# Kernel optimization log

Measured on AMD Instinct MI355X. Metric: run time of the kernel, lower is better.

## Reference

```python
import jax, jax.numpy as jnp
import numpy as np

N_NODES = 50000
N_EDGES = 800000
IN, N1, N2, N3, N4, N5, L, NC = 7, 128, 128, 64, 64, 16, 16, 3


def _gat_params(key, fin, fout, edge_dim=1):
    ks = jax.random.split(key, 6)
    s = 0.1
    return dict(
        W=jax.random.normal(ks[0], (fin, fout), jnp.float32) * s,
        a_src=jax.random.normal(ks[1], (fout,), jnp.float32) * s,
        a_dst=jax.random.normal(ks[2], (fout,), jnp.float32) * s,
        We=jax.random.normal(ks[3], (edge_dim, fout), jnp.float32) * s,
        a_e=jax.random.normal(ks[4], (fout,), jnp.float32) * s,
        b=jax.random.normal(ks[5], (fout,), jnp.float32) * s,
    )


def setup_inputs() -> dict:
    key = jax.random.key(0)
    ks = jax.random.split(key, 16)
    inp = {
        'x1': jax.random.normal(ks[0], (N_NODES, IN), jnp.float32),
        'x2': jax.random.normal(ks[1], (N_NODES, IN), jnp.float32),
        'edge_index1': jax.random.randint(ks[2], (2, N_EDGES), 0, N_NODES),
        'edge_index2': jax.random.randint(ks[3], (2, N_EDGES), 0, N_NODES),
        'x_norm2_1': jax.random.normal(ks[4], (L,), jnp.float32),
        'x_norm2_2': jax.random.normal(ks[5], (L,), jnp.float32),
        'edge_col1': jax.random.uniform(ks[6], (N_EDGES, 1), jnp.float32),
        'edge_col2': jax.random.uniform(ks[7], (N_EDGES, 1), jnp.float32),
    }
    p1 = _gat_params(ks[8], IN, N1)
    p2 = _gat_params(ks[9], N1, N2)
    p3 = _gat_params(ks[10], N2, N3)
    for i, p in enumerate((p1, p2, p3), 1):
        for k, v in p.items():
            inp[f'{k}{i}'] = v
    s = 0.1
    inp['W_lin'] = jax.random.normal(ks[11], (N3 + L, N4), jnp.float32) * s
    inp['b_lin'] = jnp.zeros((N4,), jnp.float32)
    inp['W_c1'] = jax.random.normal(ks[12], (2 * N4, N5), jnp.float32) * s
    inp['b_c1'] = jnp.zeros((N5,), jnp.float32)
    inp['W_c2'] = jax.random.normal(ks[13], (N5, NC), jnp.float32) * s
    inp['b_c2'] = jnp.zeros((NC,), jnp.float32)
    return inp


def _gat_conv(x, src, dst, eattr, W, a_src, a_dst, We, a_e, b, n):
    # PyG GATConv, heads=1, add_self_loops with fill_value='mean'
    h = x @ W                                           # [N, C]
    ones = jnp.ones_like(dst, dtype=eattr.dtype)
    deg = jax.ops.segment_sum(ones, dst, n)
    loop_attr = jax.ops.segment_sum(eattr, dst, n) / jnp.maximum(deg, 1.0)[:, None]
    ar = jnp.arange(n, dtype=src.dtype)
    s = jnp.concatenate([src, ar])
    d = jnp.concatenate([dst, ar])
    ea = jnp.concatenate([eattr, loop_attr], axis=0)    # [E+N, edge_dim]
    alpha = (h @ a_src)[s] + (h @ a_dst)[d] + (ea @ We) @ a_e
    alpha = jax.nn.leaky_relu(alpha, 0.2)
    amax = jax.ops.segment_max(alpha, d, n)             # every node has a self loop
    ex = jnp.exp(alpha - amax[d])
    denom = jax.ops.segment_sum(ex, d, n)
    w = ex / denom[d]                                   # segment softmax weights
    out = jax.ops.segment_sum(w[:, None] * h[s], d, n)  # [N, C]
    return out + b


def _process_graph(x, ei, eattr, params):
    src, dst = ei[0], ei[1]
    n = x.shape[0]
    for p in params:
        x = jax.nn.elu(_gat_conv(x, src, dst, eattr, *p, n))
    return x.mean(axis=0)


def reference(x1, x2, edge_index1, edge_index2, x_norm2_1, x_norm2_2,
              edge_col1, edge_col2,
              W1, a_src1, a_dst1, We1, a_e1, b1,
              W2, a_src2, a_dst2, We2, a_e2, b2,
              W3, a_src3, a_dst3, We3, a_e3, b3,
              W_lin, b_lin, W_c1, b_c1, W_c2, b_c2):
    params = [
        (W1, a_src1, a_dst1, We1, a_e1, b1),
        (W2, a_src2, a_dst2, We2, a_e2, b2),
        (W3, a_src3, a_dst3, We3, a_e3, b3),
    ]
    g1 = _process_graph(x1, edge_index1, edge_col1, params)
    g2 = _process_graph(x2, edge_index2, edge_col2, params)
    g1 = jnp.concatenate([g1, x_norm2_1]) @ W_lin + b_lin
    g2 = jnp.concatenate([g2, x_norm2_2]) @ W_lin + b_lin
    x = jnp.concatenate([g1, g2])                       # [2*N4]
    h = jax.nn.relu(x @ W_c1 + b_c1)
    logits = h @ W_c2 + b_c2
    return logits[None, :]                              # [1, num_classes]
```

## Files before the change

### kernel.cpp

```cpp
#include <hip/hip_runtime.h>
#include <math.h>

#define NN 50000
#define NE 800000
#define NT 100000
#define NTP 100032
#define ET (2*NE + NT)
#define NPB 256
#define NB 391
#define BCH 4096
#define BCAP 5120

typedef __attribute__((ext_vector_type(8))) short bf16x8;
typedef __attribute__((ext_vector_type(4))) float f32x4;

static __device__ __forceinline__ float wave_max64(float v){
  #pragma unroll
  for(int off=32;off;off>>=1) v = fmaxf(v, __shfl_xor(v,off));
  return v;
}
static __device__ __forceinline__ float wave_sum64(float v){
  #pragma unroll
  for(int off=32;off;off>>=1) v += __shfl_xor(v,off);
  return v;
}
static __device__ __forceinline__ unsigned short f2bf(float f){
  unsigned u = __float_as_uint(f);
  return (unsigned short)((u + 0x7FFFu + ((u>>16)&1u)) >> 16);
}
static __device__ __forceinline__ float bflo(unsigned v){ return __uint_as_float(v<<16); }
static __device__ __forceinline__ float bfhi(unsigned v){ return __uint_as_float(v & 0xFFFF0000u); }

__global__ __launch_bounds__(256) void k_hist(const int* __restrict__ d1,
    const int* __restrict__ d2, int* __restrict__ bcnt){
  __shared__ int h[512];
  int t = threadIdx.x;
  h[t] = 0; h[t+256] = 0;
  __syncthreads();
  int stride = gridDim.x*256;
  for (int e = blockIdx.x*256 + t; e < NE; e += stride){
    atomicAdd(&h[d1[e]>>8], 1);
    atomicAdd(&h[(d2[e]+NN)>>8], 1);
  }
  __syncthreads();
  if (h[t])     atomicAdd(&bcnt[t],     h[t]);
  if (h[t+256]) atomicAdd(&bcnt[t+256], h[t+256]);
}

__global__ void k_hscan(const int* __restrict__ bcnt, int* __restrict__ hbase,
                        int* __restrict__ row_ptr){
  int t = threadIdx.x;
  int a = bcnt[2*t], b2 = bcnt[2*t+1];
  int s = a + b2;
  int lane = t & 63, wv = t >> 6;
  int inc = s;
  #pragma unroll
  for (int off=1; off<64; off<<=1){ int u = __shfl_up(inc, off); if (lane>=off) inc += u; }
  __shared__ int wsum[4];
  if (lane==63) wsum[wv] = inc;
  __syncthreads();
  int woff = 0;
  #pragma unroll
  for (int w=0; w<4; ++w) if (w < wv) woff += wsum[w];
  int excl = woff + inc - s;
  hbase[2*t] = excl; hbase[2*t+1] = excl + a;
  if (t==0) row_ptr[NT] = ET;
}

__global__ __launch_bounds__(256) void k_bin(const int* __restrict__ s1,
    const int* __restrict__ d1, const float* __restrict__ e1,
    const int* __restrict__ s2, const int* __restrict__ d2,
    const float* __restrict__ e2, const int* __restrict__ hbase,
    int* __restrict__ gcur, uint2* __restrict__ gstage){
  __shared__ int cnt[512], loff[512], cur[512], gbase_sh[512];
  __shared__ uint2 sdata[BCH];
  __shared__ unsigned short sbkt[BCH];
  __shared__ int wsum[4];
  int tid = threadIdx.x;
  int e0 = blockIdx.x*BCH;
  unsigned pack[16], eab[16];
  unsigned short bk[16];
  cnt[tid] = 0; cnt[tid+256] = 0; cur[tid] = 0; cur[tid+256] = 0;
  __syncthreads();
  #pragma unroll
  for (int u=0; u<16; ++u){
    int e = e0 + u*256 + tid;
    int b = NB; unsigned p = 0, ea = 0;
    if (e < 2*NE){
      int src, dst; float eav;
      if (e < NE){ src = s1[e]; dst = d1[e]; eav = e1[e]; }
      else { int e2i = e - NE; src = s2[e2i] + NN; dst = d2[e2i] + NN; eav = e2[e2i]; }
      b = dst >> 8;
      p = (unsigned)src | ((unsigned)(dst & 255) << 17);
      ea = __float_as_uint(eav);
    }
    bk[u] = (unsigned short)b; pack[u] = p; eab[u] = ea;
    atomicAdd(&cnt[b], 1);
  }
  __syncthreads();
  {
    int a = cnt[2*tid], b2 = cnt[2*tid+1];
    int s = a + b2;
    int lane = tid & 63, wv = tid >> 6;
    int inc = s;
    #pragma unroll
    for (int off=1; off<64; off<<=1){ int u = __shfl_up(inc, off); if (lane>=off) inc += u; }
    if (lane==63) wsum[wv] = inc;
    __syncthreads();
    int woff = 0;
    #pragma unroll
    for (int w=0; w<4; ++w) if (w < wv) woff += wsum[w];
    int excl = woff + inc - s;
    loff[2*tid] = excl; loff[2*tid+1] = excl + a;
  }
  if (tid < NB && cnt[tid] > 0)
    gbase_sh[tid] = hbase[tid] + atomicAdd(&gcur[tid], cnt[tid]);
  if (tid+256 < NB && cnt[tid+256] > 0)
    gbase_sh[tid+256] = hbase[tid+256] + atomicAdd(&gcur[tid+256], cnt[tid+256]);
  __syncthreads();
  #pragma unroll
  for (int u=0; u<16; ++u){
    int b = bk[u];
    int p = loff[b] + atomicAdd(&cur[b], 1);
    sdata[p] = make_uint2(pack[u], eab[u]);
    sbkt[p] = (unsigned short)b;
  }
  __syncthreads();
  for (int k = tid; k < BCH; k += 256){
    int b = sbkt[k];
    if (b < NB) gstage[gbase_sh[b] + (k - loff[b])] = sdata[k];
  }
}

__global__ __launch_bounds__(256) void k_bucket(const uint2* __restrict__ gstage,
    const int* __restrict__ hbase, int2* __restrict__ srt, int* __restrict__ row_ptr){
  __shared__ uint2 sd[BCAP];
  __shared__ int deg[256], rbase[256], cur[256];
  __shared__ float easum[256];
  __shared__ int wsum[4];
  int b = blockIdx.x, t = threadIdx.x;
  int lo = b*NPB;
  int nloc = min(NPB, NT - lo);
  int est = hbase[b], ecnt = hbase[b+1] - est;
  bool inlds = (ecnt <= BCAP);
  deg[t] = 0; easum[t] = 0.f;
  __syncthreads();
  for (int k = t; k < ecnt; k += 256){
    uint2 v = gstage[est + k];
    if (inlds) sd[k] = v;
    int dl = v.x >> 17;
    atomicAdd(&deg[dl], 1);
    atomicAdd(&easum[dl], __uint_as_float(v.y));
  }
  __syncthreads();
  int dv = (t < nloc) ? deg[t] + 1 : 0;
  int lane = t & 63, wv = t >> 6;
  int inc = dv;
  #pragma unroll
  for (int off=1; off<64; off<<=1){ int u = __shfl_up(inc, off); if (lane>=off) inc += u; }
  if (lane==63) wsum[wv] = inc;
  __syncthreads();
  int woff = 0;
  #pragma unroll
  for (int w=0; w<4; ++w) if (w < wv) woff += wsum[w];
  int gb = est + lo + (woff + inc - dv);
  if (t < nloc){
    row_ptr[lo + t] = gb;
    rbase[t] = gb;
    cur[t] = 1;
    float se = easum[t] / fmaxf((float)deg[t], 1.f);
    srt[gb] = make_int2(lo + t, __float_as_int(se));
  }
  __syncthreads();
  for (int k = t; k < ecnt; k += 256){
    uint2 v = inlds ? sd[k] : gstage[est + k];
    int dl = v.x >> 17;
    int pos = rbase[dl] + atomicAdd(&cur[dl], 1);
    srt[pos] = make_int2((int)(v.x & 0x1FFFFu), (int)v.y);
  }
}

__global__ __launch_bounds__(256) void k_prep(
    const float* __restrict__ We0, const float* __restrict__ ae0,
    const float* __restrict__ We1, const float* __restrict__ ae1,
    const float* __restrict__ We2, const float* __restrict__ ae2,
    float* __restrict__ ce3,
    const float* __restrict__ W1, const float* __restrict__ W2,
    unsigned short* __restrict__ Wt1, unsigned short* __restrict__ Wt2){
  int t = threadIdx.x;
  if (t < 64){
    const float* We[3] = {We0, We1, We2};
    const float* ae[3] = {ae0, ae1, ae2};
    const int fo[3] = {128, 128, 64};
    for (int L = 0; L < 3; ++L){
      float s = 0.f;
      for (int c = t; c < fo[L]; c += 64) s += We[L][c]*ae[L][c];
      s = wave_sum64(s);
      if (t == 0) ce3[L] = s;
    }
  }
  for (int i = t; i < 128*128; i += 256){
    int c = i >> 7, k = i & 127;
    Wt1[c*136 + k] = f2bf(W1[k*128 + c]);
  }
  for (int i = t; i < 64*128; i += 256){
    int c = i >> 7, k = i & 127;
    Wt2[c*136 + k] = f2bf(W2[k*64 + c]);
  }
}

template<int N>
__global__ __launch_bounds__(256) void k_gemm_mfma(
    const unsigned short* __restrict__ x16, const unsigned short* __restrict__ Wt,
    const float* __restrict__ a_src, const float* __restrict__ a_dst,
    unsigned short* __restrict__ h16, float* __restrict__ hs,
    float* __restrict__ hd, int n){
  constexpr int CT = N/16;
  __shared__ unsigned short Wl[N*136];
  int tid = threadIdx.x;
  for (int i = tid; i < N*136/8; i += 256)
    ((uint4*)Wl)[i] = ((const uint4*)Wt)[i];
  __syncthreads();
  int lane = tid & 63, w = tid >> 6;
  int arow = blockIdx.x*64 + w*16 + (lane & 15);
  int kb   = (lane >> 4) * 8;
  int rsafe = (arow < n) ? arow : (n-1);
  f32x4 acc[CT] = {};
  #pragma unroll
  for (int s = 0; s < 4; ++s){
    bf16x8 a = *(const bf16x8*)(x16 + (size_t)rsafe*128 + s*32 + kb);
    #pragma unroll
    for (int c = 0; c < CT; ++c){
      bf16x8 b = *(const bf16x8*)(&Wl[(c*16 + (lane&15))*136 + s*32 + kb]);
      acc[c] = __builtin_amdgcn_mfma_f32_16x16x32_bf16(a, b, acc[c], 0, 0, 0);
    }
  }
  int drow = blockIdx.x*64 + w*16 + (lane>>4)*4;
  int dcol = lane & 15;
  float psv[4] = {0,0,0,0}, pdv[4] = {0,0,0,0};
  #pragma unroll
  for (int c = 0; c < CT; ++c){
    float as = a_src[c*16 + dcol], ad = a_dst[c*16 + dcol];
    #pragma unroll
    for (int j = 0; j < 4; ++j){
      float v = acc[c][j];
      if (drow + j < n) h16[(size_t)(drow+j)*N + c*16 + dcol] = f2bf(v);
      psv[j] += v*as; pdv[j] += v*ad;
    }
  }
  #pragma unroll
  for (int off = 1; off < 16; off <<= 1){
    #pragma unroll
    for (int j=0;j<4;j++){ psv[j] += __shfl_xor(psv[j], off); pdv[j] += __shfl_xor(pdv[j], off); }
  }
  if (dcol == 0){
    #pragma unroll
    for (int j=0;j<4;j++) if (drow+j < n){ hs[drow+j] = psv[j]; hd[drow+j] = pdv[j]; }
  }
}

__global__ __launch_bounds__(256) void k_gemm7(const float* __restrict__ x1,
    const float* __restrict__ x2, const float* __restrict__ W,
    const float* __restrict__ a_src, const float* __restrict__ a_dst,
    unsigned short* __restrict__ h16, float* __restrict__ hs,
    float* __restrict__ hd, int n){
  __shared__ float Wl[7][128];
  int tid = threadIdx.x;
  for (int i = tid; i < 7*128; i += 256) ((float*)Wl)[i] = W[i];
  __syncthreads();
  int tx = tid & 31, ty = tid >> 5;
  int r = blockIdx.x*8 + ty;
  if (r >= n) return;
  const float* xr = (r < NN) ? (x1 + (size_t)r*7) : (x2 + (size_t)(r-NN)*7);
  float xv[7];
  #pragma unroll
  for (int k=0;k<7;k++) xv[k] = xr[k];
  float4 s = make_float4(0.f,0.f,0.f,0.f);
  #pragma unroll
  for (int k=0;k<7;k++){
    float4 wv = *(const float4*)(&Wl[k][tx*4]);
    s.x += xv[k]*wv.x; s.y += xv[k]*wv.y; s.z += xv[k]*wv.z; s.w += xv[k]*wv.w;
  }
  unsigned r0p = (unsigned)f2bf(s.x) | ((unsigned)f2bf(s.y)<<16);
  unsigned r1p = (unsigned)f2bf(s.z) | ((unsigned)f2bf(s.w)<<16);
  *(uint2*)(h16 + (size_t)r*128 + tx*4) = make_uint2(r0p, r1p);
  float ps = s.x*a_src[tx*4] + s.y*a_src[tx*4+1] + s.z*a_src[tx*4+2] + s.w*a_src[tx*4+3];
  float pd = s.x*a_dst[tx*4] + s.y*a_dst[tx*4+1] + s.z*a_dst[tx*4+2] + s.w*a_dst[tx*4+3];
  #pragma unroll
  for (int off=16; off; off>>=1){ ps += __shfl_xor(ps, off); pd += __shfl_xor(pd, off); }
  if (tx==0){ hs[r] = ps; hd[r] = pd; }
}

template<int FOUT, bool OBF>
__global__ __launch_bounds__(256) void k_aggregate(const unsigned short* __restrict__ h16,
    const float* __restrict__ hs, const float* __restrict__ hd,
    const int2* __restrict__ srt, const int* __restrict__ row_ptr,
    const float* __restrict__ ce_p, const float* __restrict__ b,
    void* __restrict__ xout, int n){
  constexpr int LPE = FOUT/8;
  constexpr int EPS = 64/LPE;
  __shared__ float s_p[4][64];
  __shared__ int   s_s[4][64];
  int tid = threadIdx.x;
  int wv = tid >> 6, lane = tid & 63;
  int wid = (int)((blockIdx.x*256 + tid) >> 6);
  if (wid >= n) return;
  float ce  = *ce_p;
  int beg = row_ptr[wid], end = row_ptr[wid+1];
  float hdn = hd[wid];
  int e_sub = lane / LPE;
  int col8  = (lane % LPE) * 8;
  float m = -INFINITY, den = 0.f;
  float acc[8] = {0.f,0.f,0.f,0.f,0.f,0.f,0.f,0.f};
  for (int base = beg; base < end; base += 64){
    int slot = base + lane;
    float a = -INFINITY; int src = 0;
    if (slot < end){
      int2 pk = srt[slot];
      src = pk.x;
      a = hs[src] + hdn + __int_as_float(pk.y)*ce;
      a = (a > 0.f) ? a : 0.2f*a;
    }
    float cm = wave_max64(a);
    float mnew = fmaxf(m, cm);
    float scale = __expf(m - mnew);
    den *= scale;
    #pragma unroll
    for (int u=0;u<8;u++) acc[u] *= scale;
    float p = __expf(a - mnew);
    den += wave_sum64(p);
    s_p[wv][lane] = p; s_s[wv][lane] = src;
    asm volatile("s_waitcnt lgkmcnt(0)" ::: "memory");
    int cnt = end - base; if (cnt > 64) cnt = 64;
    for (int j = 0; j < cnt; j += EPS){
      int jj = j + e_sub;
      float p0 = s_p[wv][jj];  int sj = s_s[wv][jj];
      uint4 h0 = *(const uint4*)(h16 + (size_t)sj*FOUT + col8);
      acc[0] += p0*bflo(h0.x); acc[1] += p0*bfhi(h0.x);
      acc[2] += p0*bflo(h0.y); acc[3] += p0*bfhi(h0.y);
      acc[4] += p0*bflo(h0.z); acc[5] += p0*bfhi(h0.z);
      acc[6] += p0*bflo(h0.w); acc[7] += p0*bfhi(h0.w);
    }
    m = mnew;
  }
  #pragma unroll
  for (int off = LPE; off < 64; off <<= 1){
    #pragma unroll
    for (int u=0;u<8;u++) acc[u] += __shfl_xor(acc[u], off);
  }
  float inv = 1.f/den;
  if (lane < LPE){
    float o[8];
    #pragma unroll
    for (int u=0;u<8;u++){
      o[u] = acc[u]*inv + b[col8+u];
      o[u] = (o[u] > 0.f) ? o[u] : (__expf(o[u]) - 1.f);
    }
    if (OBF){
      uint4 pkd;
      pkd.x = (unsigned)f2bf(o[0]) | ((unsigned)f2bf(o[1])<<16);
      pkd.y = (unsigned)f2bf(o[2]) | ((unsigned)f2bf(o[3])<<16);
      pkd.z = (unsigned)f2bf(o[4]) | ((unsigned)f2bf(o[5])<<16);
      pkd.w = (unsigned)f2bf(o[6]) | ((unsigned)f2bf(o[7])<<16);
      *(uint4*)((unsigned short*)xout + (size_t)wid*FOUT + col8) = pkd;
    } else {
      float4 o0 = make_float4(o[0],o[1],o[2],o[3]);
      float4 o1 = make_float4(o[4],o[5],o[6],o[7]);
      *(float4*)((float*)xout + (size_t)wid*FOUT + col8)     = o0;
      *(float4*)((float*)xout + (size_t)wid*FOUT + col8 + 4) = o1;
    }
  }
}

__global__ __launch_bounds__(256) void k_colsum2(const float* __restrict__ x,
    float* __restrict__ gsum, int n){
  __shared__ float ls[128];
  int t = threadIdx.x;
  if (t < 128) ls[t] = 0.f;
  __syncthreads();
  int c4 = (t & 15) * 4;
  int rsub = t >> 4;
  float4 s1 = make_float4(0.f,0.f,0.f,0.f), s2 = make_float4(0.f,0.f,0.f,0.f);
  for (int r = blockIdx.x*16 + rsub; r < n; r += gridDim.x*16){
    float4 v = *(const float4*)(x + (size_t)r*64 + c4);
    if (r < NN){ s1.x+=v.x; s1.y+=v.y; s1.z+=v.z; s1.w+=v.w; }
    else       { s2.x+=v.x; s2.y+=v.y; s2.z+=v.z; s2.w+=v.w; }
  }
  atomicAdd(&ls[c4+0], s1.x); atomicAdd(&ls[c4+1], s1.y);
  atomicAdd(&ls[c4+2], s1.z); atomicAdd(&ls[c4+3], s1.w);
  atomicAdd(&ls[64+c4+0], s2.x); atomicAdd(&ls[64+c4+1], s2.y);
  atomicAdd(&ls[64+c4+2], s2.z); atomicAdd(&ls[64+c4+3], s2.w);
  __syncthreads();
  if (t < 128) atomicAdd(&gsum[t], ls[t]);
}

__global__ void k_head(const float* __restrict__ gs1, const float* __restrict__ gs2,
                       const float* __restrict__ xn1, const float* __restrict__ xn2,
                       const float* __restrict__ Wlin, const float* __restrict__ blin,
                       const float* __restrict__ Wc1, const float* __restrict__ bc1,
                       const float* __restrict__ Wc2, const float* __restrict__ bc2,
                       float* __restrict__ out){
  __shared__ float c1[80], c2[80], xcat[128], hb[16];
  int tid = threadIdx.x;
  const float invn = 1.f/(float)NN;
  if (tid < 64){ c1[tid] = gs1[tid]*invn; c2[tid] = gs2[tid]*invn; }
  else if (tid < 80){ c1[tid] = xn1[tid-64]; c2[tid] = xn2[tid-64]; }
  __syncthreads();
  if (tid < 64){
    float s = blin[tid];
    for (int k=0;k<80;k++) s += c1[k]*Wlin[k*64+tid];
    xcat[tid] = s;
  } else {
    int j = tid - 64;
    float s = blin[j];
    for (int k=0;k<80;k++) s += c2[k]*Wlin[k*64+j];
    xcat[tid] = s;
  }
  __syncthreads();
  if (tid < 16){
    float s = bc1[tid];
    for (int k=0;k<128;k++) s += xcat[k]*Wc1[k*16+tid];
    hb[tid] = fmaxf(s, 0.f);
  }
  __syncthreads();
  if (tid < 3){
    float s = bc2[tid];
    for (int k=0;k<16;k++) s += hb[k]*Wc2[k*3+tid];
    out[tid] = s;
  }
}

extern "C" void kernel_launch(void* const* d_in, const int* in_sizes, int n_in,
                              void* d_out, int out_size, void* d_ws, size_t ws_size,
                              hipStream_t stream){
  const float* x1  = (const float*)d_in[0];
  const float* x2  = (const float*)d_in[1];
  const int*   ei1 = (const int*)d_in[2];
  const int*   ei2 = (const int*)d_in[3];
  const float* xn1 = (const float*)d_in[4];
  const float* xn2 = (const float*)d_in[5];
  const float* ec1 = (const float*)d_in[6];
  const float* ec2 = (const float*)d_in[7];
  const float* W[3]    = {(const float*)d_in[8],  (const float*)d_in[14], (const float*)d_in[20]};
  const float* asrc[3] = {(const float*)d_in[9],  (const float*)d_in[15], (const float*)d_in[21]};
  const float* adst[3] = {(const float*)d_in[10], (const float*)d_in[16], (const float*)d_in[22]};
  const float* We[3]   = {(const float*)d_in[11], (const float*)d_in[17], (const float*)d_in[23]};
  const float* ae[3]   = {(const float*)d_in[12], (const float*)d_in[18], (const float*)d_in[24]};
  const float* bb[3]   = {(const float*)d_in[13], (const float*)d_in[19], (const float*)d_in[25]};
  const float* Wlin = (const float*)d_in[26];
  const float* blin = (const float*)d_in[27];
  const float* Wc1  = (const float*)d_in[28];
  const float* bc1  = (const float*)d_in[29];
  const float* Wc2  = (const float*)d_in[30];
  const float* bc2  = (const float*)d_in[31];
  float* out = (float*)d_out;

  char* wsb = (char*)d_ws;
  unsigned short* x16   = (unsigned short*)wsb;
  uint2*          gstage = (uint2*)wsb;
  float*          bufX  = (float*)wsb;
  unsigned short* h16  = (unsigned short*)(wsb + (size_t)NTP*128*2);
  int2*           srt  = (int2*)(wsb + (size_t)NTP*128*2 + (size_t)NT*128*2);
  float* hs   = (float*)(srt + ET);
  float* hd   = hs + NT;
  int*   row_ptr = (int*)(hd + NT);
  int*   bcnt  = row_ptr + NT + 2;
  int*   gcur  = bcnt + 512;
  float* gsum  = (float*)(gcur + 512);
  int*   hbase = (int*)(gsum + 128);
  float* ce3   = (float*)(hbase + 513);
  unsigned short* Wt1 = (unsigned short*)(ce3 + 8);
  unsigned short* Wt2 = Wt1 + 128*136;

  const int* s1 = ei1, * d1 = ei1 + NE;
  const int* s2 = ei2, * d2 = ei2 + NE;

  hipMemsetAsync(bcnt, 0, (512+512+128)*sizeof(int), stream);
  k_prep<<<1, 256, 0, stream>>>(We[0], ae[0], We[1], ae[1], We[2], ae[2], ce3,
                                W[1], W[2], Wt1, Wt2);

  k_hist<<<256, 256, 0, stream>>>(d1, d2, bcnt);
  k_hscan<<<1, 256, 0, stream>>>(bcnt, hbase, row_ptr);
  k_bin<<<(2*NE + BCH - 1)/BCH, 256, 0, stream>>>(s1, d1, ec1, s2, d2, ec2, hbase, gcur, gstage);
  k_bucket<<<NB, 256, 0, stream>>>(gstage, hbase, srt, row_ptr);

  k_gemm7<<<(NT+7)/8, 256, 0, stream>>>(x1, x2, W[0], asrc[0], adst[0], h16, hs, hd, NT);
  k_aggregate<128,true><<<(NT+3)/4, 256, 0, stream>>>(h16, hs, hd, srt, row_ptr, ce3+0, bb[0], x16, NT);
  k_gemm_mfma<128><<<(NT+63)/64, 256, 0, stream>>>(x16, Wt1, asrc[1], adst[1], h16, hs, hd, NT);
  k_aggregate<128,true><<<(NT+3)/4, 256, 0, stream>>>(h16, hs, hd, srt, row_ptr, ce3+1, bb[1], x16, NT);
  k_gemm_mfma<64><<<(NT+63)/64, 256, 0, stream>>>(x16, Wt2, asrc[2], adst[2], h16, hs, hd, NT);
  k_aggregate<64,false><<<(NT+3)/4, 256, 0, stream>>>(h16, hs, hd, srt, row_ptr, ce3+2, bb[2], bufX, NT);

  k_colsum2<<<512, 256, 0, stream>>>(bufX, gsum, NT);
  k_head<<<1, 128, 0, stream>>>(gsum, gsum+64, xn1, xn2, Wlin, blin, Wc1, bc1, Wc2, bc2, out);
}
```

Baseline: 475.4 us.

## Halve sort bucket size, fuse counter zeroing into prep, unroll aggregation gather

Edge sorting now uses 128-node buckets instead of 256, giving 782 buckets with smaller per-block chunks. The histogram, scan, bin and bucket kernels are reworked to handle the larger bucket count. This is meant to spread the bucket pass over more blocks with less shared memory each, at the cost of more global atomics and bookkeeping. The separate memset is removed and the counters are zeroed inside k_prep instead. The aggregation inner loop is unrolled by two so two neighbor feature loads can be in flight at once, which adds register pressure.

Measured after the change: 457.5 us. -3.8%, faster.

```diff
diff --git a/kernel.cpp b/kernel.cpp
--- a/kernel.cpp
+++ b/kernel.cpp
@@ -6,10 +6,10 @@
 #define NT 100000
 #define NTP 100032
 #define ET (2*NE + NT)
-#define NPB 256
-#define NB 391
-#define BCH 4096
-#define BCAP 5120
+#define NPB 128
+#define NBK 782
+#define BCH 2048
+#define BCAP 2816
 
 typedef __attribute__((ext_vector_type(8))) short bf16x8;
 typedef __attribute__((ext_vector_type(4))) float f32x4;
@@ -33,27 +33,32 @@
 
 __global__ __launch_bounds__(256) void k_hist(const int* __restrict__ d1,
     const int* __restrict__ d2, int* __restrict__ bcnt){
-  __shared__ int h[512];
+  __shared__ int h[1024];
   int t = threadIdx.x;
-  h[t] = 0; h[t+256] = 0;
+  #pragma unroll
+  for (int i=0;i<4;i++) h[t + i*256] = 0;
   __syncthreads();
   int stride = gridDim.x*256;
   for (int e = blockIdx.x*256 + t; e < NE; e += stride){
-    atomicAdd(&h[d1[e]>>8], 1);
-    atomicAdd(&h[(d2[e]+NN)>>8], 1);
-  }
-  __syncthreads();
-  if (h[t])     atomicAdd(&bcnt[t],     h[t]);
-  if (h[t+256]) atomicAdd(&bcnt[t+256], h[t+256]);
+    atomicAdd(&h[d1[e]>>7], 1);
+    atomicAdd(&h[(d2[e]+NN)>>7], 1);
+  }
+  __syncthreads();
+  #pragma unroll
+  for (int i=0;i<4;i++){
+    int idx = t + i*256;
+    if (h[idx]) atomicAdd(&bcnt[idx], h[idx]);
+  }
 }
 
 __global__ void k_hscan(const int* __restrict__ bcnt, int* __restrict__ hbase,
                         int* __restrict__ row_ptr){
   int t = threadIdx.x;
-  int a = bcnt[2*t], b2 = bcnt[2*t+1];
-  int s = a + b2;
+  int i0 = t*4;
+  int c0=bcnt[i0], c1=bcnt[i0+1], c2=bcnt[i0+2], c3=bcnt[i0+3];
+  int ts = c0+c1+c2+c3;
   int lane = t & 63, wv = t >> 6;
-  int inc = s;
+  int inc = ts;
   #pragma unroll
   for (int off=1; off<64; off<<=1){ int u = __shfl_up(inc, off); if (lane>=off) inc += u; }
   __shared__ int wsum[4];
@@ -62,8 +67,8 @@
   int woff = 0;
   #pragma unroll
   for (int w=0; w<4; ++w) if (w < wv) woff += wsum[w];
-  int excl = woff + inc - s;
-  hbase[2*t] = excl; hbase[2*t+1] = excl + a;
+  int run = woff + inc - ts;
+  hbase[i0] = run; hbase[i0+1] = run+c0; hbase[i0+2] = run+c0+c1; hbase[i0+3] = run+c0+c1+c2;
   if (t==0) row_ptr[NT] = ET;
 }
 
@@ -72,26 +77,27 @@
     const int* __restrict__ s2, const int* __restrict__ d2,
     const float* __restrict__ e2, const int* __restrict__ hbase,
     int* __restrict__ gcur, uint2* __restrict__ gstage){
-  __shared__ int cnt[512], loff[512], cur[512], gbase_sh[512];
+  __shared__ int cnt[1024], loff[1024], cur[1024], gbase_sh[1024];
   __shared__ uint2 sdata[BCH];
   __shared__ unsigned short sbkt[BCH];
   __shared__ int wsum[4];
   int tid = threadIdx.x;
   int e0 = blockIdx.x*BCH;
-  unsigned pack[16], eab[16];
-  unsigned short bk[16];
-  cnt[tid] = 0; cnt[tid+256] = 0; cur[tid] = 0; cur[tid+256] = 0;
-  __syncthreads();
-  #pragma unroll
-  for (int u=0; u<16; ++u){
+  unsigned pack[8], eab[8];
+  unsigned short bk[8];
+  #pragma unroll
+  for (int i=0;i<4;i++){ cnt[tid + i*256] = 0; cur[tid + i*256] = 0; }
+  __syncthreads();
+  #pragma unroll
+  for (int u=0; u<8; ++u){
     int e = e0 + u*256 + tid;
-    int b = NB; unsigned p = 0, ea = 0;
+    int b = NBK; unsigned p = 0, ea = 0;
     if (e < 2*NE){
       int src, dst; float eav;
       if (e < NE){ src = s1[e]; dst = d1[e]; eav = e1[e]; }
       else { int e2i = e - NE; src = s2[e2i] + NN; dst = d2[e2i] + NN; eav = e2[e2i]; }
-      b = dst >> 8;
-      p = (unsigned)src | ((unsigned)(dst & 255) << 17);
+      b = dst >> 7;
+      p = (unsigned)src | ((unsigned)(dst & 127) << 17);
       ea = __float_as_uint(eav);
     }
     bk[u] = (unsigned short)b; pack[u] = p; eab[u] = ea;
@@ -99,10 +105,11 @@
   }
   __syncthreads();
   {
-    int a = cnt[2*tid], b2 = cnt[2*tid+1];
-    int s = a + b2;
+    int i0 = tid*4;
+    int c0=cnt[i0], c1=cnt[i0+1], c2=cnt[i0+2], c3=cnt[i0+3];
+    int ts = c0+c1+c2+c3;
     int lane = tid & 63, wv = tid >> 6;
-    int inc = s;
+    int inc = ts;
     #pragma unroll
     for (int off=1; off<64; off<<=1){ int u = __shfl_up(inc, off); if (lane>=off) inc += u; }
     if (lane==63) wsum[wv] = inc;
@@ -110,16 +117,14 @@
     int woff = 0;
     #pragma unroll
     for (int w=0; w<4; ++w) if (w < wv) woff += wsum[w];
-    int excl = woff + inc - s;
-    loff[2*tid] = excl; loff[2*tid+1] = excl + a;
-  }
-  if (tid < NB && cnt[tid] > 0)
-    gbase_sh[tid] = hbase[tid] + atomicAdd(&gcur[tid], cnt[tid]);
-  if (tid+256 < NB && cnt[tid+256] > 0)
-    gbase_sh[tid+256] = hbase[tid+256] + atomicAdd(&gcur[tid+256], cnt[tid+256]);
-  __syncthreads();
-  #pragma unroll
-  for (int u=0; u<16; ++u){
+    int run = woff + inc - ts;
+    loff[i0] = run; loff[i0+1] = run+c0; loff[i0+2] = run+c0+c1; loff[i0+3] = run+c0+c1+c2;
+  }
+  for (int i = tid; i < NBK; i += 256)
+    if (cnt[i] > 0) gbase_sh[i] = hbase[i] + atomicAdd(&gcur[i], cnt[i]);
+  __syncthreads();
+  #pragma unroll
+  for (int u=0; u<8; ++u){
     int b = bk[u];
     int p = loff[b] + atomicAdd(&cur[b], 1);
     sdata[p] = make_uint2(pack[u], eab[u]);
@@ -128,22 +133,22 @@
   __syncthreads();
   for (int k = tid; k < BCH; k += 256){
     int b = sbkt[k];
-    if (b < NB) gstage[gbase_sh[b] + (k - loff[b])] = sdata[k];
+    if (b < NBK) gstage[gbase_sh[b] + (k - loff[b])] = sdata[k];
   }
 }
 
 __global__ __launch_bounds__(256) void k_bucket(const uint2* __restrict__ gstage,
     const int* __restrict__ hbase, int2* __restrict__ srt, int* __restrict__ row_ptr){
   __shared__ uint2 sd[BCAP];
-  __shared__ int deg[256], rbase[256], cur[256];
-  __shared__ float easum[256];
+  __shared__ int deg[NPB], rbase[NPB], cur[NPB];
+  __shared__ float easum[NPB];
   __shared__ int wsum[4];
   int b = blockIdx.x, t = threadIdx.x;
   int lo = b*NPB;
   int nloc = min(NPB, NT - lo);
   int est = hbase[b], ecnt = hbase[b+1] - est;
   bool inlds = (ecnt <= BCAP);
-  deg[t] = 0; easum[t] = 0.f;
+  if (t < NPB){ deg[t] = 0; easum[t] = 0.f; }
   __syncthreads();
   for (int k = t; k < ecnt; k += 256){
     uint2 v = gstage[est + k];
@@ -184,10 +189,11 @@
     const float* __restrict__ We0, const float* __restrict__ ae0,
     const float* __restrict__ We1, const float* __restrict__ ae1,
     const float* __restrict__ We2, const float* __restrict__ ae2,
-    float* __restrict__ ce3,
+    float* __restrict__ ce3, int* __restrict__ zbase,
     const float* __restrict__ W1, const float* __restrict__ W2,
     unsigned short* __restrict__ Wt1, unsigned short* __restrict__ Wt2){
   int t = threadIdx.x;
+  for (int i = t; i < 1024+1024+128; i += 256) zbase[i] = 0;
   if (t < 64){
     const float* We[3] = {We0, We1, We2};
     const float* ae[3] = {ae0, ae1, ae2};
@@ -332,14 +338,20 @@
     s_p[wv][lane] = p; s_s[wv][lane] = src;
     asm volatile("s_waitcnt lgkmcnt(0)" ::: "memory");
     int cnt = end - base; if (cnt > 64) cnt = 64;
-    for (int j = 0; j < cnt; j += EPS){
-      int jj = j + e_sub;
-      float p0 = s_p[wv][jj];  int sj = s_s[wv][jj];
-      uint4 h0 = *(const uint4*)(h16 + (size_t)sj*FOUT + col8);
+    for (int j = 0; j < cnt; j += 2*EPS){
+      int jj0 = j + e_sub, jj1 = j + EPS + e_sub;
+      float p0 = s_p[wv][jj0];  int sj0 = s_s[wv][jj0];
+      float p1 = s_p[wv][jj1];  int sj1 = s_s[wv][jj1];
+      uint4 h0 = *(const uint4*)(h16 + (size_t)sj0*FOUT + col8);
+      uint4 h1 = *(const uint4*)(h16 + (size_t)sj1*FOUT + col8);
       acc[0] += p0*bflo(h0.x); acc[1] += p0*bfhi(h0.x);
       acc[2] += p0*bflo(h0.y); acc[3] += p0*bfhi(h0.y);
       acc[4] += p0*bflo(h0.z); acc[5] += p0*bfhi(h0.z);
       acc[6] += p0*bflo(h0.w); acc[7] += p0*bfhi(h0.w);
+      acc[0] += p1*bflo(h1.x); acc[1] += p1*bfhi(h1.x);
+      acc[2] += p1*bflo(h1.y); acc[3] += p1*bfhi(h1.y);
+      acc[4] += p1*bflo(h1.z); acc[5] += p1*bfhi(h1.z);
+      acc[6] += p1*bflo(h1.w); acc[7] += p1*bfhi(h1.w);
     }
     m = mnew;
   }
@@ -465,24 +477,23 @@
   float* hd   = hs + NT;
   int*   row_ptr = (int*)(hd + NT);
   int*   bcnt  = row_ptr + NT + 2;
-  int*   gcur  = bcnt + 512;
-  float* gsum  = (float*)(gcur + 512);
+  int*   gcur  = bcnt + 1024;
+  float* gsum  = (float*)(gcur + 1024);
   int*   hbase = (int*)(gsum + 128);
-  float* ce3   = (float*)(hbase + 513);
+  float* ce3   = (float*)(hbase + 1024);
   unsigned short* Wt1 = (unsigned short*)(ce3 + 8);
   unsigned short* Wt2 = Wt1 + 128*136;
 
   const int* s1 = ei1, * d1 = ei1 + NE;
   const int* s2 = ei2, * d2 = ei2 + NE;
 
-  hipMemsetAsync(bcnt, 0, (512+512+128)*sizeof(int), stream);
   k_prep<<<1, 256, 0, stream>>>(We[0], ae[0], We[1], ae[1], We[2], ae[2], ce3,
-                                W[1], W[2], Wt1, Wt2);
+                                bcnt, W[1], W[2], Wt1, Wt2);
 
   k_hist<<<256, 256, 0, stream>>>(d1, d2, bcnt);
   k_hscan<<<1, 256, 0, stream>>>(bcnt, hbase, row_ptr);
   k_bin<<<(2*NE + BCH - 1)/BCH, 256, 0, stream>>>(s1, d1, ec1, s2, d2, ec2, hbase, gcur, gstage);
-  k_bucket<<<NB, 256, 0, stream>>>(gstage, hbase, srt, row_ptr);
+  k_bucket<<<NBK, 256, 0, stream>>>(gstage, hbase, srt, row_ptr);
 
   k_gemm7<<<(NT+7)/8, 256, 0, stream>>>(x1, x2, W[0], asrc[0], adst[0], h16, hs, hd, NT);
   k_aggregate<128,true><<<(NT+3)/4, 256, 0, stream>>>(h16, hs, hd, srt, row_ptr, ce3+0, bb[0], x16, NT);
```
